# Optimization experiments

Hardware: AMD Instinct MI355X
Metric: run time of the kernel (lower is better)

Reference implementation:

```python
import jax, jax.numpy as jnp
import numpy as np

H = 768       # hidden_size
HEADS = 8     # num_heads
T = 3         # num_timesteps
B = 128       # molecules in batch
N_ATOM = 48   # atoms per molecule
E_INTRA = 96  # intra-molecule directed edges per molecule
NPG = N_ATOM + 1          # nodes per graph (incl. virtual)
EPG = E_INTRA + N_ATOM    # edges per graph (incl. atom->virtual)
N = B * NPG
E = B * EPG


def setup_inputs() -> dict:
    key = jax.random.key(0)
    ks = jax.random.split(key, 10)
    atom_feat = jax.random.normal(ks[0], (B, N_ATOM, H), dtype=jnp.float32)
    mol_feat = jax.random.normal(ks[1], (B, H), dtype=jnp.float32)
    # node features with virtual node (=mol_feat) appended per graph, as in add_virtual_nodes_and_edges
    h_nodes = jnp.concatenate([atom_feat, mol_feat[:, None, :]], axis=1).reshape(N, H)
    off = jnp.arange(B, dtype=jnp.int32) * NPG
    intra_src = jax.random.randint(ks[2], (B, E_INTRA), 0, N_ATOM, dtype=jnp.int32) + off[:, None]
    intra_dst = jax.random.randint(ks[3], (B, E_INTRA), 0, N_ATOM, dtype=jnp.int32) + off[:, None]
    virt_src = jnp.arange(N_ATOM, dtype=jnp.int32)[None, :] + off[:, None]
    virt_dst = jnp.broadcast_to((off + N_ATOM)[:, None], (B, N_ATOM))
    src = jnp.concatenate([intra_src, virt_src], axis=1).reshape(E)
    dst = jnp.concatenate([intra_dst, virt_dst], axis=1).reshape(E)
    virtual_nids = off + N_ATOM  # last node of each graph (cumsum(batch_num_nodes)-1)
    attn_eids = ((jnp.arange(B, dtype=jnp.int32) * EPG)[:, None]
                 + E_INTRA + jnp.arange(N_ATOM, dtype=jnp.int32)[None, :]).reshape(-1)
    s = 0.02
    W_src = jax.random.normal(ks[4], (T, H, HEADS * H), dtype=jnp.float32) * s
    W_dst = jax.random.normal(ks[5], (T, H, HEADS * H), dtype=jnp.float32) * s
    attn_a = jax.random.normal(ks[6], (T, HEADS, H), dtype=jnp.float32) * s
    W_ih = jax.random.normal(ks[7], (T, 3 * H, H), dtype=jnp.float32) * s
    W_hh = jax.random.normal(ks[8], (T, 3 * H, H), dtype=jnp.float32) * s
    b_src = jnp.zeros((T, HEADS * H), jnp.float32)
    b_dst = jnp.zeros((T, HEADS * H), jnp.float32)
    b_ih = jnp.zeros((T, 3 * H), jnp.float32)
    b_hh = jnp.zeros((T, 3 * H), jnp.float32)
    return {"h_nodes": h_nodes, "mol_feat": mol_feat, "W_src": W_src, "b_src": b_src,
            "W_dst": W_dst, "b_dst": b_dst, "attn_a": attn_a, "W_ih": W_ih, "W_hh": W_hh,
            "b_ih": b_ih, "b_hh": b_hh, "src": src, "dst": dst,
            "virtual_nids": virtual_nids, "attn_eids": attn_eids}


def _gru_cell(x, hprev, W_ih_t, W_hh_t, b_ih_t, b_hh_t):
    # torch.nn.GRUCell: gates ordered r, z, n
    gi = x @ W_ih_t.T + b_ih_t
    gh = hprev @ W_hh_t.T + b_hh_t
    ir, iz, inn = jnp.split(gi, 3, axis=-1)
    hr, hz, hn = jnp.split(gh, 3, axis=-1)
    r = jax.nn.sigmoid(ir + hr)
    z = jax.nn.sigmoid(iz + hz)
    n = jnp.tanh(inn + r * hn)
    return (1.0 - z) * n + z * hprev


def _forward(h_nodes, mol_feat, W_src, b_src, W_dst, b_dst, attn_a,
             W_ih, W_hh, b_ih, b_hh, src, dst, virtual_nids, attn_eids):
    h = h_nodes
    mol_emb = mol_feat
    attns = []
    for t in range(T):
        # GATv2Conv (DGL, eval mode so feat_drop/attn_drop are identity)
        fs = (h @ W_src[t] + b_src[t]).reshape(N, HEADS, H)
        fd = (h @ W_dst[t] + b_dst[t]).reshape(N, HEADS, H)
        e = jax.nn.leaky_relu(fs[src] + fd[dst], negative_slope=0.2)  # [E, heads, H]
        logits = jnp.einsum('ehd,hd->eh', e, attn_a[t])               # [E, heads]
        # edge softmax over incoming edges per destination node
        m = jax.ops.segment_max(logits, dst, num_segments=N)
        ex = jnp.exp(logits - m[dst])
        ssum = jax.ops.segment_sum(ex, dst, num_segments=N)
        a = ex / ssum[dst]                                            # [E, heads]
        rst = jax.ops.segment_sum(a[:, :, None] * fs[src], dst, num_segments=N)  # [N, heads, H]
        h = rst.mean(axis=1)                                          # mean over heads
        out_virtual = h[virtual_nids]                                 # [B, H]
        mol_emb = jax.nn.relu(_gru_cell(out_virtual, mol_emb, W_ih[t], W_hh[t], b_ih[t], b_hh[t]))
        attns.append(a.mean(axis=1)[attn_eids])                       # attention on virtual edges
    return mol_emb, jnp.stack(attns)


def reference(h_nodes, mol_feat, W_src, b_src, W_dst, b_dst, attn_a,
              W_ih, W_hh, b_ih, b_hh, src, dst, virtual_nids, attn_eids):
    return _forward(h_nodes, mol_feat, W_src, b_src, W_dst, b_dst, attn_a,
                    W_ih, W_hh, b_ih, b_hh, src, dst, virtual_nids, attn_eids)
```

## Files before the change

### kernel.cpp

```cpp
#include <hip/hip_runtime.h>
#include <hip/hip_bf16.h>

typedef __hip_bfloat16 bf16;
typedef float f32x4 __attribute__((ext_vector_type(4)));
typedef __bf16 bf16x8 __attribute__((ext_vector_type(8)));
typedef short s16x8 __attribute__((ext_vector_type(8)));
typedef short s16x2 __attribute__((ext_vector_type(2)));

#define HDIM 768
#define NHEAD 8
#define BMOL 128
#define NPG 49
#define EPG 144
#define NNODE (BMOL * NPG)
#define NEDGE (BMOL * EPG)
#define NH 6144
#define G3 2304

__device__ __forceinline__ float b2f(short s) {
    unsigned int u = ((unsigned int)(unsigned short)s) << 16;
    return __builtin_bit_cast(float, u);
}

__device__ __forceinline__ void async16(const bf16* g, bf16* l) {
    __builtin_amdgcn_global_load_lds(
        (const __attribute__((address_space(1))) void*)g,
        (__attribute__((address_space(3))) void*)l, 16, 0, 0);
}

#define VMCNT(n) asm volatile("s_waitcnt vmcnt(" #n ")" ::: "memory")
#define SBAR()                                 \
    do {                                       \
        asm volatile("" ::: "memory");         \
        __builtin_amdgcn_s_barrier();          \
        asm volatile("" ::: "memory");         \
    } while (0)

__global__ __launch_bounds__(512, 2) void gemm_bt8(
    const bf16* __restrict__ A, const bf16* __restrict__ Bt0,
    const bf16* __restrict__ Bt1, const float* __restrict__ bias0,
    const float* __restrict__ bias1, bf16* __restrict__ C0,
    bf16* __restrict__ C1) {
    __shared__ __align__(16) char smem[131072];
    bf16* lA = (bf16*)smem;
    bf16* lB = (bf16*)(smem + 65536);

    const int tid = threadIdx.x;
    const int lane = tid & 63;
    const int wave = tid >> 6;
    const int l16 = lane & 15;
    const int quad = lane >> 4;
    const int wm = wave >> 2;
    const int wn = wave & 3;
    const int K = HDIM;

    int id = blockIdx.y * 24 + blockIdx.x;
    const int xcd = id & 7;
    const int loc = id >> 3;
    const int mc = loc / 15;
    const int rem = loc % 15;
    const int ncol = rem / 5;
    const int moff = rem % 5;
    const int m0 = (mc * 5 + moff) * 256;
    const int n0 = (xcd * 3 + ncol) * 256;

    const bf16* Bt = blockIdx.z ? Bt1 : Bt0;
    const float* bias = blockIdx.z ? bias1 : bias0;
    bf16* C = blockIdx.z ? C1 : C0;

    const int srow = tid >> 3;
    const int ecol =
        ((tid & 7) * 8) ^ ((srow & 1) * 32) ^ ((srow & 2) * 8);
    const bf16* gAr[4];
#pragma unroll
    for (int hc = 0; hc < 4; ++hc) {
        int r = m0 + srow + hc * 64;
        if (r > NNODE - 1) r = NNODE - 1;
        gAr[hc] = A + (size_t)r * K + ecol;
    }
    const bf16* gB = Bt + (size_t)(n0 + srow) * K + ecol;
    const size_t hstep = (size_t)128 * K;
    const size_t cstep = (size_t)64 * K;
    bf16* dA = lA + tid * 8;
    bf16* dB = lB + tid * 8;

#define STAGE_A(buf, h, kt)                                     \
    do {                                                        \
        bf16* _d = dA + (buf)*16384 + (h)*8192;                 \
        async16(gAr[(h)*2] + (size_t)(kt) * 64, _d);            \
        async16(gAr[(h)*2 + 1] + (size_t)(kt) * 64, _d + 4096); \
    } while (0)
#define STAGE_B(buf, h, kt)                                     \
    do {                                                        \
        const bf16* _s = gB + (h)*hstep + (size_t)(kt) * 64;    \
        bf16* _d = dB + (buf)*16384 + (h)*8192;                 \
        async16(_s, _d);                                        \
        async16(_s + cstep, _d + 4096);                         \
    } while (0)

    const int q16 = quad * 16;
    const int sw = ((l16 & 1) << 6) | ((l16 & 2) << 4);
    const char* laRow = (const char*)lA + wm * 16384 + l16 * 128;
    const char* lbRow =
        (const char*)lB + (wn >> 1) * 16384 + (wn & 1) * 8192 + l16 * 128;

#define LDA8(buf, f, ks) \
    (*(const bf16x8*)(laRow + (buf)*32768 + (f)*2048 + ((q16 + (ks)*64) ^ sw)))
#define LDB8(buf, j, ks) \
    (*(const bf16x8*)(lbRow + (buf)*32768 + (j)*2048 + ((q16 + (ks)*64) ^ sw)))

    f32x4 acc[8][4];
#pragma unroll
    for (int i = 0; i < 8; ++i)
#pragma unroll
        for (int j = 0; j < 4; ++j) acc[i][j] = (f32x4){0.f, 0.f, 0.f, 0.f};
    bf16x8 bfr[4][2];

#define MF(i, j, ks, areg)                                             \
    acc[i][j] = __builtin_amdgcn_mfma_f32_16x16x32_bf16(areg, bfr[j][ks], \
                                                        acc[i][j], 0, 0, 0)

#define PHASE(buf, q, LB, STG, WAIT)                                   \
    do {                                                               \
        bf16x8 a00 = LDA8(buf, (q)*2, 0);                              \
        bf16x8 a01 = LDA8(buf, (q)*2, 1);                              \
        bf16x8 a10 = LDA8(buf, (q)*2 + 1, 0);                          \
        bf16x8 a11 = LDA8(buf, (q)*2 + 1, 1);                          \
        if (LB) {                                                      \
            bfr[0][0] = LDB8(buf, 0, 0); bfr[0][1] = LDB8(buf, 0, 1);  \
            bfr[1][0] = LDB8(buf, 1, 0); bfr[1][1] = LDB8(buf, 1, 1);  \
            bfr[2][0] = LDB8(buf, 2, 0); bfr[2][1] = LDB8(buf, 2, 1);  \
            bfr[3][0] = LDB8(buf, 3, 0); bfr[3][1] = LDB8(buf, 3, 1);  \
        }                                                              \
        STG;                                                           \
        SBAR();                                                        \
        __builtin_amdgcn_s_setprio(1);                                 \
        MF((q)*2, 0, 0, a00); MF((q)*2, 1, 0, a00);                    \
        MF((q)*2, 2, 0, a00); MF((q)*2, 3, 0, a00);                    \
        MF((q)*2 + 1, 0, 0, a10); MF((q)*2 + 1, 1, 0, a10);            \
        MF((q)*2 + 1, 2, 0, a10); MF((q)*2 + 1, 3, 0, a10);            \
        MF((q)*2, 0, 1, a01); MF((q)*2, 1, 1, a01);                    \
        MF((q)*2, 2, 1, a01); MF((q)*2, 3, 1, a01);                    \
        MF((q)*2 + 1, 0, 1, a11); MF((q)*2 + 1, 1, 1, a11);            \
        MF((q)*2 + 1, 2, 1, a11); MF((q)*2 + 1, 3, 1, a11);            \
        __builtin_amdgcn_s_setprio(0);                                 \
        WAIT;                                                          \
        SBAR();                                                        \
    } while (0)

    STAGE_A(0, 0, 0); STAGE_A(0, 1, 0);
    STAGE_B(0, 0, 0); STAGE_B(0, 1, 0);
    STAGE_B(1, 0, 1); STAGE_B(1, 1, 1);
    VMCNT(4);
    SBAR();

    int t0 = 0;
    for (int it = 0; it < 5; ++it, t0 += 2) {
        PHASE(0, 0, 1, STAGE_A(1, 0, t0 + 1), );
        PHASE(0, 1, 0, STAGE_A(1, 1, t0 + 1), );
        PHASE(0, 2, 0, STAGE_B(0, 0, t0 + 2), );
        PHASE(0, 3, 0, STAGE_B(0, 1, t0 + 2), VMCNT(4));
        PHASE(1, 0, 1, STAGE_A(0, 0, t0 + 2), );
        PHASE(1, 1, 0, STAGE_A(0, 1, t0 + 2), );
        PHASE(1, 2, 0, STAGE_B(1, 0, t0 + 3), );
        PHASE(1, 3, 0, STAGE_B(1, 1, t0 + 3), VMCNT(4));
    }
    PHASE(0, 0, 1, STAGE_A(1, 0, 11), );
    PHASE(0, 1, 0, STAGE_A(1, 1, 11), );
    PHASE(0, 2, 0, , );
    PHASE(0, 3, 0, , VMCNT(0));
    PHASE(1, 0, 1, , );
    PHASE(1, 1, 0, , );
    PHASE(1, 2, 0, , );
    PHASE(1, 3, 0, , );

    __syncthreads();
#pragma unroll
    for (int i = 0; i < 8; ++i) {
        const int rloc = wm * 128 + i * 16 + quad * 4;
#pragma unroll
        for (int j = 0; j < 4; ++j) {
            const int cloc = wn * 64 + j * 16 + l16;
            const float bc = bias[n0 + cloc];
#pragma unroll
            for (int r = 0; r < 4; ++r) {
                const int rr = rloc + r;
                int off = (rr * 512 + cloc * 2) ^ ((rr & 4) ? 32 : 0);
                *(bf16*)(smem + off) = __float2bfloat16(acc[i][j][r] + bc);
            }
        }
    }
    __syncthreads();
#pragma unroll
    for (int k = 0; k < 16; ++k) {
        const int off = (k * 512 + tid) * 16;
        const int row = off >> 9;
        const int bcol = (off & 511) ^ ((row & 4) ? 32 : 0);
        if (m0 + row < NNODE) {
            bf16x8 v = *(const bf16x8*)(smem + off);
            *(bf16x8*)(C + (size_t)(m0 + row) * NH + n0 + (bcol >> 1)) = v;
        }
    }
#undef PHASE
#undef MF
#undef LDA8
#undef LDB8
#undef STAGE_A
#undef STAGE_B
}

__global__ __launch_bounds__(256) void gemm_small(
    const bf16* __restrict__ hws, const int* __restrict__ vnids,
    const bf16* __restrict__ A1, const bf16* __restrict__ B0,
    const bf16* __restrict__ B1, const float* __restrict__ bias0,
    const float* __restrict__ bias1, float* __restrict__ C0,
    float* __restrict__ C1) {
    __shared__ __align__(16) bf16 lA[32 * 32];
    __shared__ __align__(16) bf16 lB[256 * 32];
    const int tid = threadIdx.x;
    const int lane = tid & 63;
    const int wave = tid >> 6;
    const int l16 = lane & 15;
    const int quad = lane >> 4;
    const int K = HDIM;
    const int y0 = blockIdx.y * 32;
    const int x0 = blockIdx.x * 256;
    const bf16* Bt = blockIdx.z ? B1 : B0;
    const float* bias = blockIdx.z ? bias1 : bias0;
    float* C = blockIdx.z ? C1 : C0;

    const int ry = y0 + (tid >> 2);
    const bf16* gA;
    if (blockIdx.z)
        gA = A1 + (size_t)ry * K + (tid & 3) * 8;
    else
        gA = hws + (size_t)vnids[ry & 127] * K + (tid & 3) * 8;
    const bf16* gB = Bt + (size_t)(x0 + (tid >> 2)) * K + (tid & 3) * 8;
    bf16* lAp = lA + tid * 8;
    bf16* lBp = lB + tid * 8;
    const size_t rstep = (size_t)64 * K;

    f32x4 acc[2][4];
#pragma unroll
    for (int i = 0; i < 2; ++i)
#pragma unroll
        for (int j = 0; j < 4; ++j) acc[i][j] = (f32x4){0.f, 0.f, 0.f, 0.f};

    for (int k0 = 0; k0 < K; k0 += 32) {
        __syncthreads();
        if (tid < 128) async16(gA + k0, lAp);
        async16(gB + k0, lBp);
        async16(gB + k0 + rstep, lBp + 2048);
        async16(gB + k0 + 2 * rstep, lBp + 4096);
        async16(gB + k0 + 3 * rstep, lBp + 6144);
        __syncthreads();
        bf16x8 af[2], bfr[4];
#pragma unroll
        for (int i = 0; i < 2; ++i)
            af[i] = *(const bf16x8*)(lA + (i * 16 + l16) * 32 + quad * 8);
#pragma unroll
        for (int j = 0; j < 4; ++j)
            bfr[j] = *(const bf16x8*)(lB + (wave * 64 + j * 16 + l16) * 32 +
                                      quad * 8);
#pragma unroll
        for (int i = 0; i < 2; ++i)
#pragma unroll
            for (int j = 0; j < 4; ++j)
                acc[i][j] = __builtin_amdgcn_mfma_f32_16x16x32_bf16(
                    af[i], bfr[j], acc[i][j], 0, 0, 0);
    }

#pragma unroll
    for (int i = 0; i < 2; ++i) {
#pragma unroll
        for (int j = 0; j < 4; ++j) {
            int row = y0 + i * 16 + quad * 4;
            int col = x0 + wave * 64 + j * 16 + l16;
            float bc = bias[col];
#pragma unroll
            for (int r = 0; r < 4; ++r)
                C[(size_t)(row + r) * G3 + col] = acc[i][j][r] + bc;
        }
    }
}

__global__ __launch_bounds__(256) void transpose_w(
    const float* __restrict__ W, bf16* __restrict__ Wt, int K, int Nn) {
    __shared__ bf16 tile[64][65];
    const int z = blockIdx.z;
    const float* Wp = W + (size_t)z * K * Nn;
    bf16* Wtp = Wt + (size_t)z * K * Nn;
    const int n0 = blockIdx.x * 64;
    const int k0 = blockIdx.y * 64;
    const int tx = threadIdx.x & 63;
    const int ty = threadIdx.x >> 6;
#pragma unroll
    for (int i = 0; i < 64; i += 4)
        tile[ty + i][tx] = __float2bfloat16(Wp[(size_t)(k0 + ty + i) * Nn + n0 + tx]);
    __syncthreads();
#pragma unroll
    for (int i = 0; i < 64; i += 4)
        Wtp[(size_t)(n0 + ty + i) * K + k0 + tx] = tile[tx][ty + i];
}

__global__ void cvt_kernel(const float* __restrict__ x, bf16* __restrict__ y,
                           int n) {
    int i = blockIdx.x * 256 + threadIdx.x;
    if (i < n) y[i] = __float2bfloat16(x[i]);
}

__global__ __launch_bounds__(256) void logits_kernel(
    const bf16* __restrict__ fs, const bf16* __restrict__ fd,
    const float* __restrict__ attn_a_t, const int* __restrict__ src,
    const int* __restrict__ dst, float* __restrict__ logits) {
    __shared__ __align__(16) float s_a[NH];
    const int tid = threadIdx.x;
    for (int p = tid; p < NH; p += 256) s_a[p] = attn_a_t[p];
    __syncthreads();

    const int wave = tid >> 6;
    const int lane = tid & 63;
    const int e = blockIdx.x * 4 + wave;
    const int gs = src[e], gd = dst[e];
    const bf16* ps = fs + (size_t)gs * NH;
    const bf16* pd = fd + (size_t)gd * NH;
    const int h = lane >> 3;
    const int s = lane & 7;
    const int base = h * HDIM + s * 8;

    float acc = 0.f;
#pragma unroll
    for (int j = 0; j < 12; ++j) {
        const int off = base + j * 64;
        s16x8 a8 = *(const s16x8*)(ps + off);
        s16x8 d8 = *(const s16x8*)(pd + off);
        f32x4 av0 = *(const f32x4*)(s_a + off);
        f32x4 av1 = *(const f32x4*)(s_a + off + 4);
#pragma unroll
        for (int u = 0; u < 4; ++u) {
            float x = b2f(a8[u]) + b2f(d8[u]);
            x = (x > 0.f) ? x : 0.2f * x;
            acc += x * av0[u];
        }
#pragma unroll
        for (int u = 0; u < 4; ++u) {
            float x = b2f(a8[4 + u]) + b2f(d8[4 + u]);
            x = (x > 0.f) ? x : 0.2f * x;
            acc += x * av1[u];
        }
    }
    acc += __shfl_xor(acc, 1);
    acc += __shfl_xor(acc, 2);
    acc += __shfl_xor(acc, 4);
    if (s == 0) logits[(size_t)e * NHEAD + h] = acc;
}

__global__ __launch_bounds__(256) void softmax_kernel(
    const float* __restrict__ logits, const int* __restrict__ dst,
    float* __restrict__ w, float* __restrict__ outv) {
    __shared__ float s_logit[EPG * NHEAD];
    __shared__ float s_w[EPG * NHEAD];
    __shared__ int s_ld[EPG];
    __shared__ float s_m[NPG * NHEAD], s_inv[NPG * NHEAD];
    const int tid = threadIdx.x;
    const int b = blockIdx.x;
    for (int p = tid; p < EPG * NHEAD; p += 256)
        s_logit[p] = logits[(size_t)b * EPG * NHEAD + p];
    if (tid < EPG) s_ld[tid] = dst[b * EPG + tid] - b * NPG;
    __syncthreads();

    for (int p = tid; p < NPG * NHEAD; p += 256) {
        int n = p >> 3, h = p & 7;
        float m = -3.0e38f;
        for (int le = 0; le < EPG; ++le)
            if (s_ld[le] == n) m = fmaxf(m, s_logit[le * NHEAD + h]);
        float ss = 0.f;
        for (int le = 0; le < EPG; ++le)
            if (s_ld[le] == n) ss += __expf(s_logit[le * NHEAD + h] - m);
        s_m[p] = m;
        s_inv[p] = (ss > 0.f) ? 1.f / ss : 0.f;
    }
    __syncthreads();

    for (int p = tid; p < EPG * NHEAD; p += 256) {
        int le = p >> 3, h = p & 7;
        int ld = s_ld[le];
        float a =
            0.125f * __expf(s_logit[p] - s_m[ld * NHEAD + h]) * s_inv[ld * NHEAD + h];
        s_w[p] = a;
        w[(size_t)b * EPG * NHEAD + p] = a;
    }
    __syncthreads();
    if (tid < 48) {
        float s = 0.f;
#pragma unroll
        for (int h = 0; h < NHEAD; ++h) s += s_w[(96 + tid) * NHEAD + h];
        outv[b * 48 + tid] = s;
    }
}

__global__ __launch_bounds__(256) void aggregate_kernel(
    const bf16* __restrict__ fs, const float* __restrict__ w,
    const int* __restrict__ src, const int* __restrict__ dst,
    bf16* __restrict__ hout) {
    __shared__ float acc[NPG * 128];
    __shared__ float s_w[EPG * NHEAD];
    __shared__ int s_gs[EPG], s_ld[EPG];
    const int tid = threadIdx.x;
    const int c = blockIdx.x;
    const int b = blockIdx.y;
    const int grp = tid >> 6;
    const int l = tid & 63;
    if (tid < EPG) {
        int e = b * EPG + tid;
        s_gs[tid] = src[e];
        s_ld[tid] = dst[e] - b * NPG;
    }
    for (int p = tid; p < EPG * NHEAD; p += 256)
        s_w[p] = w[(size_t)b * EPG * NHEAD + p];
    for (int p = tid; p < NPG * 128; p += 256) acc[p] = 0.f;
    __syncthreads();

    const int dim = c * 128 + l * 2;
    for (int le4 = 0; le4 < EPG; le4 += 4) {
        const int le = le4 + grp;
        const bf16* p = fs + (size_t)s_gs[le] * NH + dim;
        float sum0 = 0.f, sum1 = 0.f;
#pragma unroll
        for (int h = 0; h < NHEAD; ++h) {
            s16x2 v = *(const s16x2*)(p + h * HDIM);
            float wv = s_w[le * NHEAD + h];
            sum0 += wv * b2f(v[0]);
            sum1 += wv * b2f(v[1]);
        }
        float* ap = &acc[s_ld[le] * 128 + l * 2];
        atomicAdd(ap, sum0);
        atomicAdd(ap + 1, sum1);
    }
    __syncthreads();
    for (int p = tid; p < NPG * 128; p += 256) {
        int n = p >> 7, d = p & 127;
        hout[((size_t)b * NPG + n) * HDIM + c * 128 + d] =
            __float2bfloat16(acc[p]);
    }
}

__global__ void init_memb_kernel(const float* __restrict__ mf,
                                 float* __restrict__ m32,
                                 bf16* __restrict__ m16) {
    int idx = blockIdx.x * 256 + threadIdx.x;
    float f = mf[idx];
    m32[idx] = f;
    m16[idx] = __float2bfloat16(f);
}

__global__ void gru_gate_kernel(const float* __restrict__ gi,
                                const float* __restrict__ gh,
                                float* __restrict__ m32, bf16* __restrict__ m16,
                                float* __restrict__ outp, int last) {
    int idx = blockIdx.x * 256 + threadIdx.x;
    int b = idx / HDIM, d = idx - b * HDIM;
    const float* gib = gi + (size_t)b * G3;
    const float* ghb = gh + (size_t)b * G3;
    float ir = gib[d], iz = gib[HDIM + d], in_ = gib[2 * HDIM + d];
    float hr = ghb[d], hz = ghb[HDIM + d], hn = ghb[2 * HDIM + d];
    float r = 1.f / (1.f + __expf(-(ir + hr)));
    float z = 1.f / (1.f + __expf(-(iz + hz)));
    float n = tanhf(in_ + r * hn);
    float hprev = m32[idx];
    float hnew = (1.f - z) * n + z * hprev;
    hnew = fmaxf(hnew, 0.f);
    m32[idx] = hnew;
    m16[idx] = __float2bfloat16(hnew);
    if (last) outp[idx] = hnew;
}

extern "C" void kernel_launch(void* const* d_in, const int* in_sizes, int n_in,
                              void* d_out, int out_size, void* d_ws,
                              size_t ws_size, hipStream_t stream) {
    const float* h_nodes = (const float*)d_in[0];
    const float* mol_feat = (const float*)d_in[1];
    const float* W_src = (const float*)d_in[2];
    const float* b_src = (const float*)d_in[3];
    const float* W_dst = (const float*)d_in[4];
    const float* b_dst = (const float*)d_in[5];
    const float* attn_a = (const float*)d_in[6];
    const float* W_ih = (const float*)d_in[7];
    const float* W_hh = (const float*)d_in[8];
    const float* b_ih = (const float*)d_in[9];
    const float* b_hh = (const float*)d_in[10];
    const int* src = (const int*)d_in[11];
    const int* dst = (const int*)d_in[12];
    const int* vnids = (const int*)d_in[13];
    float* out = (float*)d_out;

    char* p = (char*)d_ws;
    auto alloc = [&](size_t bytes) {
        char* r = p;
        p += (bytes + 255) & ~(size_t)255;
        return r;
    };
    bf16* wsrcT = (bf16*)alloc((size_t)3 * NH * HDIM * 2);
    bf16* wdstT = (bf16*)alloc((size_t)3 * NH * HDIM * 2);
    bf16* wihB = (bf16*)alloc((size_t)3 * G3 * HDIM * 2);
    bf16* whhB = (bf16*)alloc((size_t)3 * G3 * HDIM * 2);
    bf16* fs = (bf16*)alloc((size_t)NNODE * NH * 2);
    bf16* fd = (bf16*)alloc((size_t)NNODE * NH * 2);
    bf16* h_ws = (bf16*)alloc((size_t)NNODE * HDIM * 2);
    float* lg = (float*)alloc((size_t)NEDGE * NHEAD * 4);
    float* w_e = (float*)alloc((size_t)NEDGE * NHEAD * 4);
    float* memb32 = (float*)alloc((size_t)BMOL * HDIM * 4);
    bf16* memb16 = (bf16*)alloc((size_t)BMOL * HDIM * 2);
    float* gi = (float*)alloc((size_t)BMOL * G3 * 4);
    float* gh = (float*)alloc((size_t)BMOL * G3 * 4);

    dim3 tgrid(NH / 64, HDIM / 64, 3);
    transpose_w<<<tgrid, 256, 0, stream>>>(W_src, wsrcT, HDIM, NH);
    transpose_w<<<tgrid, 256, 0, stream>>>(W_dst, wdstT, HDIM, NH);
    {
        int n = 3 * G3 * HDIM;
        cvt_kernel<<<(n + 255) / 256, 256, 0, stream>>>(W_ih, wihB, n);
        cvt_kernel<<<(n + 255) / 256, 256, 0, stream>>>(W_hh, whhB, n);
    }
    {
        int n = NNODE * HDIM;
        cvt_kernel<<<(n + 255) / 256, 256, 0, stream>>>(h_nodes, h_ws, n);
    }
    init_memb_kernel<<<BMOL * HDIM / 256, 256, 0, stream>>>(mol_feat, memb32,
                                                            memb16);

    for (int t = 0; t < 3; ++t) {
        gemm_bt8<<<dim3(24, 25, 2), 512, 0, stream>>>(
            h_ws, wsrcT + (size_t)t * NH * HDIM, wdstT + (size_t)t * NH * HDIM,
            b_src + (size_t)t * NH, b_dst + (size_t)t * NH, fs, fd);
        logits_kernel<<<NEDGE / 4, 256, 0, stream>>>(
            fs, fd, attn_a + (size_t)t * NHEAD * HDIM, src, dst, lg);
        softmax_kernel<<<BMOL, 256, 0, stream>>>(
            lg, dst, w_e, out + BMOL * HDIM + t * BMOL * 48);
        aggregate_kernel<<<dim3(6, BMOL), 256, 0, stream>>>(fs, w_e, src, dst,
                                                            h_ws);
        gemm_small<<<dim3(G3 / 256, 4, 2), 256, 0, stream>>>(
            h_ws, vnids, memb16, wihB + (size_t)t * G3 * HDIM,
            whhB + (size_t)t * G3 * HDIM, b_ih + (size_t)t * G3,
            b_hh + (size_t)t * G3, gi, gh);
        gru_gate_kernel<<<BMOL * HDIM / 256, 256, 0, stream>>>(
            gi, gh, memb32, memb16, out, t == 2);
    }
}
```

Before: 1.220 ms.

## Compute only virtual-node outputs in the final timestep

In the last timestep only the virtual-node outputs and the virtual-edge attention are needed. So the fd GEMM is limited to the 128 virtual nodes through a gathered GEMM. Logits, softmax and aggregation run only over the 48 atom-to-virtual edges per molecule, and the GRU input is read from a compact per-molecule buffer. This removes about half of the last step's big projection GEMM and most of its edge work, at the cost of extra specialised kernels.

```diff
diff --git a/kernel.cpp b/kernel.cpp
--- a/kernel.cpp
+++ b/kernel.cpp
@@ -214,7 +214,7 @@
     const bf16* __restrict__ A1, const bf16* __restrict__ B0,
     const bf16* __restrict__ B1, const float* __restrict__ bias0,
     const float* __restrict__ bias1, float* __restrict__ C0,
-    float* __restrict__ C1) {
+    float* __restrict__ C1, const bf16* __restrict__ A0) {
     __shared__ __align__(16) bf16 lA[32 * 32];
     __shared__ __align__(16) bf16 lB[256 * 32];
     const int tid = threadIdx.x;
@@ -233,6 +233,8 @@
     const bf16* gA;
     if (blockIdx.z)
         gA = A1 + (size_t)ry * K + (tid & 3) * 8;
+    else if (A0)
+        gA = A0 + (size_t)(ry & 127) * K + (tid & 3) * 8;
     else
         gA = hws + (size_t)vnids[ry & 127] * K + (tid & 3) * 8;
     const bf16* gB = Bt + (size_t)(x0 + (tid >> 2)) * K + (tid & 3) * 8;
@@ -280,6 +282,73 @@
 #pragma unroll
             for (int r = 0; r < 4; ++r)
                 C[(size_t)(row + r) * G3 + col] = acc[i][j][r] + bc;
+        }
+    }
+}
+
+__global__ __launch_bounds__(256) void gemm_gather_bt(
+    const bf16* __restrict__ hws, const int* __restrict__ vnids,
+    const bf16* __restrict__ Bt, const float* __restrict__ bias,
+    bf16* __restrict__ C) {
+    __shared__ __align__(16) bf16 lA[32 * 32];
+    __shared__ __align__(16) bf16 lB[256 * 32];
+    const int tid = threadIdx.x;
+    const int lane = tid & 63;
+    const int wave = tid >> 6;
+    const int l16 = lane & 15;
+    const int quad = lane >> 4;
+    const int K = HDIM;
+    const int y0 = blockIdx.y * 32;
+    const int x0 = blockIdx.x * 256;
+
+    const int ry = y0 + (tid >> 2);
+    const bf16* gA = hws + (size_t)vnids[ry & 127] * K + (tid & 3) * 8;
+    const bf16* gB = Bt + (size_t)(x0 + (tid >> 2)) * K + (tid & 3) * 8;
+    bf16* lAp = lA + tid * 8;
+    bf16* lBp = lB + tid * 8;
+    const size_t rstep = (size_t)64 * K;
+
+    f32x4 acc[2][4];
+#pragma unroll
+    for (int i = 0; i < 2; ++i)
+#pragma unroll
+        for (int j = 0; j < 4; ++j) acc[i][j] = (f32x4){0.f, 0.f, 0.f, 0.f};
+
+    for (int k0 = 0; k0 < K; k0 += 32) {
+        __syncthreads();
+        if (tid < 128) async16(gA + k0, lAp);
+        async16(gB + k0, lBp);
+        async16(gB + k0 + rstep, lBp + 2048);
+        async16(gB + k0 + 2 * rstep, lBp + 4096);
+        async16(gB + k0 + 3 * rstep, lBp + 6144);
+        __syncthreads();
+        bf16x8 af[2], bfr[4];
+#pragma unroll
+        for (int i = 0; i < 2; ++i)
+            af[i] = *(const bf16x8*)(lA + (i * 16 + l16) * 32 + quad * 8);
+#pragma unroll
+        for (int j = 0; j < 4; ++j)
+            bfr[j] = *(const bf16x8*)(lB + (wave * 64 + j * 16 + l16) * 32 +
+                                      quad * 8);
+#pragma unroll
+        for (int i = 0; i < 2; ++i)
+#pragma unroll
+            for (int j = 0; j < 4; ++j)
+                acc[i][j] = __builtin_amdgcn_mfma_f32_16x16x32_bf16(
+                    af[i], bfr[j], acc[i][j], 0, 0, 0);
+    }
+
+#pragma unroll
+    for (int i = 0; i < 2; ++i) {
+#pragma unroll
+        for (int j = 0; j < 4; ++j) {
+            int row = y0 + i * 16 + quad * 4;
+            int col = x0 + wave * 64 + j * 16 + l16;
+            float bc = bias[col];
+#pragma unroll
+            for (int r = 0; r < 4; ++r)
+                C[(size_t)(row + r) * NH + col] =
+                    __float2bfloat16(acc[i][j][r] + bc);
         }
     }
 }
@@ -355,6 +424,52 @@
     if (s == 0) logits[(size_t)e * NHEAD + h] = acc;
 }
 
+__global__ __launch_bounds__(256) void logits_virt_kernel(
+    const bf16* __restrict__ fs, const bf16* __restrict__ fdv,
+    const float* __restrict__ attn_a_t, float* __restrict__ lgv) {
+    __shared__ __align__(16) float s_a[NH];
+    const int tid = threadIdx.x;
+    for (int p = tid; p < NH; p += 256) s_a[p] = attn_a_t[p];
+    __syncthreads();
+
+    const int wave = tid >> 6;
+    const int lane = tid & 63;
+    const int e = blockIdx.x * 4 + wave;
+    const int b = e / 48;
+    const int i = e - b * 48;
+    const bf16* ps = fs + (size_t)(b * NPG + i) * NH;
+    const bf16* pd = fdv + (size_t)b * NH;
+    const int h = lane >> 3;
+    const int s = lane & 7;
+    const int base = h * HDIM + s * 8;
+
+    float acc = 0.f;
+#pragma unroll
+    for (int j = 0; j < 12; ++j) {
+        const int off = base + j * 64;
+        s16x8 a8 = *(const s16x8*)(ps + off);
+        s16x8 d8 = *(const s16x8*)(pd + off);
+        f32x4 av0 = *(const f32x4*)(s_a + off);
+        f32x4 av1 = *(const f32x4*)(s_a + off + 4);
+#pragma unroll
+        for (int u = 0; u < 4; ++u) {
+            float x = b2f(a8[u]) + b2f(d8[u]);
+            x = (x > 0.f) ? x : 0.2f * x;
+            acc += x * av0[u];
+        }
+#pragma unroll
+        for (int u = 0; u < 4; ++u) {
+            float x = b2f(a8[4 + u]) + b2f(d8[4 + u]);
+            x = (x > 0.f) ? x : 0.2f * x;
+            acc += x * av1[u];
+        }
+    }
+    acc += __shfl_xor(acc, 1);
+    acc += __shfl_xor(acc, 2);
+    acc += __shfl_xor(acc, 4);
+    if (s == 0) lgv[(size_t)e * NHEAD + h] = acc;
+}
+
 __global__ __launch_bounds__(256) void softmax_kernel(
     const float* __restrict__ logits, const int* __restrict__ dst,
     float* __restrict__ w, float* __restrict__ outv) {
@@ -399,6 +514,37 @@
     }
 }
 
+__global__ __launch_bounds__(64) void softmax_virt_kernel(
+    const float* __restrict__ lgv, float* __restrict__ wv,
+    float* __restrict__ outv) {
+    __shared__ float s_w[48 * NHEAD];
+    const int b = blockIdx.x;
+    const int tid = threadIdx.x;
+    if (tid < NHEAD) {
+        const int h = tid;
+        float m = -3.0e38f;
+        for (int i = 0; i < 48; ++i)
+            m = fmaxf(m, lgv[(size_t)(b * 48 + i) * NHEAD + h]);
+        float ss = 0.f;
+        for (int i = 0; i < 48; ++i)
+            ss += __expf(lgv[(size_t)(b * 48 + i) * NHEAD + h] - m);
+        float inv = (ss > 0.f) ? 1.f / ss : 0.f;
+        for (int i = 0; i < 48; ++i) {
+            float a =
+                0.125f * __expf(lgv[(size_t)(b * 48 + i) * NHEAD + h] - m) * inv;
+            s_w[i * NHEAD + h] = a;
+            wv[(size_t)(b * 48 + i) * NHEAD + h] = a;
+        }
+    }
+    __syncthreads();
+    if (tid < 48) {
+        float s = 0.f;
+#pragma unroll
+        for (int h = 0; h < NHEAD; ++h) s += s_w[tid * NHEAD + h];
+        outv[b * 48 + tid] = s;
+    }
+}
+
 __global__ __launch_bounds__(256) void aggregate_kernel(
     const bf16* __restrict__ fs, const float* __restrict__ w,
     const int* __restrict__ src, const int* __restrict__ dst,
@@ -443,6 +589,40 @@
         hout[((size_t)b * NPG + n) * HDIM + c * 128 + d] =
             __float2bfloat16(acc[p]);
     }
+}
+
+__global__ __launch_bounds__(256) void aggregate_virt_kernel(
+    const bf16* __restrict__ fs, const float* __restrict__ wv,
+    bf16* __restrict__ hv) {
+    __shared__ float acc[128];
+    __shared__ float s_w[48 * NHEAD];
+    const int tid = threadIdx.x;
+    const int c = blockIdx.x;
+    const int b = blockIdx.y;
+    const int grp = tid >> 6;
+    const int l = tid & 63;
+    for (int p = tid; p < 48 * NHEAD; p += 256)
+        s_w[p] = wv[(size_t)b * 48 * NHEAD + p];
+    if (tid < 128) acc[tid] = 0.f;
+    __syncthreads();
+
+    const int dim = c * 128 + l * 2;
+    float sum0 = 0.f, sum1 = 0.f;
+    for (int le = grp; le < 48; le += 4) {
+        const bf16* p = fs + (size_t)(b * NPG + le) * NH + dim;
+#pragma unroll
+        for (int h = 0; h < NHEAD; ++h) {
+            s16x2 v = *(const s16x2*)(p + h * HDIM);
+            float w_ = s_w[le * NHEAD + h];
+            sum0 += w_ * b2f(v[0]);
+            sum1 += w_ * b2f(v[1]);
+        }
+    }
+    atomicAdd(&acc[l * 2], sum0);
+    atomicAdd(&acc[l * 2 + 1], sum1);
+    __syncthreads();
+    if (tid < 128)
+        hv[(size_t)b * HDIM + c * 128 + tid] = __float2bfloat16(acc[tid]);
 }
 
 __global__ void init_memb_kernel(const float* __restrict__ mf,
@@ -530,20 +710,43 @@
                                                             memb16);
 
     for (int t = 0; t < 3; ++t) {
-        gemm_bt8<<<dim3(24, 25, 2), 512, 0, stream>>>(
-            h_ws, wsrcT + (size_t)t * NH * HDIM, wdstT + (size_t)t * NH * HDIM,
-            b_src + (size_t)t * NH, b_dst + (size_t)t * NH, fs, fd);
-        logits_kernel<<<NEDGE / 4, 256, 0, stream>>>(
-            fs, fd, attn_a + (size_t)t * NHEAD * HDIM, src, dst, lg);
-        softmax_kernel<<<BMOL, 256, 0, stream>>>(
-            lg, dst, w_e, out + BMOL * HDIM + t * BMOL * 48);
-        aggregate_kernel<<<dim3(6, BMOL), 256, 0, stream>>>(fs, w_e, src, dst,
-                                                            h_ws);
-        gemm_small<<<dim3(G3 / 256, 4, 2), 256, 0, stream>>>(
-            h_ws, vnids, memb16, wihB + (size_t)t * G3 * HDIM,
-            whhB + (size_t)t * G3 * HDIM, b_ih + (size_t)t * G3,
-            b_hh + (size_t)t * G3, gi, gh);
-        gru_gate_kernel<<<BMOL * HDIM / 256, 256, 0, stream>>>(
-            gi, gh, memb32, memb16, out, t == 2);
-    }
-}
+        if (t < 2) {
+            gemm_bt8<<<dim3(24, 25, 2), 512, 0, stream>>>(
+                h_ws, wsrcT + (size_t)t * NH * HDIM,
+                wdstT + (size_t)t * NH * HDIM, b_src + (size_t)t * NH,
+                b_dst + (size_t)t * NH, fs, fd);
+            logits_kernel<<<NEDGE / 4, 256, 0, stream>>>(
+                fs, fd, attn_a + (size_t)t * NHEAD * HDIM, src, dst, lg);
+            softmax_kernel<<<BMOL, 256, 0, stream>>>(
+                lg, dst, w_e, out + BMOL * HDIM + t * BMOL * 48);
+            aggregate_kernel<<<dim3(6, BMOL), 256, 0, stream>>>(fs, w_e, src,
+                                                                dst, h_ws);
+            gemm_small<<<dim3(G3 / 256, 4, 2), 256, 0, stream>>>(
+                h_ws, vnids, memb16, wihB + (size_t)t * G3 * HDIM,
+                whhB + (size_t)t * G3 * HDIM, b_ih + (size_t)t * G3,
+                b_hh + (size_t)t * G3, gi, gh, (const bf16*)nullptr);
+            gru_gate_kernel<<<BMOL * HDIM / 256, 256, 0, stream>>>(
+                gi, gh, memb32, memb16, out, 0);
+        } else {
+            gemm_bt8<<<dim3(24, 25, 1), 512, 0, stream>>>(
+                h_ws, wsrcT + (size_t)t * NH * HDIM,
+                wdstT + (size_t)t * NH * HDIM, b_src + (size_t)t * NH,
+                b_dst + (size_t)t * NH, fs, fd);
+            gemm_gather_bt<<<dim3(NH / 256, 4), 256, 0, stream>>>(
+                h_ws, vnids, wdstT + (size_t)t * NH * HDIM,
+                b_dst + (size_t)t * NH, fd);
+            logits_virt_kernel<<<(BMOL * 48) / 4, 256, 0, stream>>>(
+                fs, fd, attn_a + (size_t)t * NHEAD * HDIM, lg);
+            softmax_virt_kernel<<<BMOL, 64, 0, stream>>>(
+                lg, w_e, out + BMOL * HDIM + t * BMOL * 48);
+            aggregate_virt_kernel<<<dim3(6, BMOL), 256, 0, stream>>>(
+                fs, w_e, h_ws);
+            gemm_small<<<dim3(G3 / 256, 4, 2), 256, 0, stream>>>(
+                h_ws, vnids, memb16, wihB + (size_t)t * G3 * HDIM,
+                whhB + (size_t)t * G3 * HDIM, b_ih + (size_t)t * G3,
+                b_hh + (size_t)t * G3, gi, gh, h_ws);
+            gru_gate_kernel<<<BMOL * HDIM / 256, 256, 0, stream>>>(
+                gi, gh, memb32, memb16, out, 1);
+        }
+    }
+}
```

New measurement: 1.045 ms. 14.4% less time.
